# Kernel tuning notes

Measured on AMD Instinct MI355X. Metric: run time of the kernel, lower is better.

## Reference

```python
import jax, jax.numpy as jnp
import numpy as np

EPS_THRESH = 1e-10   # threshold used by GraphFilter to sparsify A
NORM_EPS = 1e-12     # torch F.normalize clamp
REG = 2.0 / 3.0      # AGE preprocess_graph reg coefficient (layer=1)


def setup_inputs() -> dict:
    key = jax.random.key(0)
    X = jax.random.normal(key, (8192, 512), dtype=jnp.float32)
    return {"X": X}


def reference(X):
    N = X.shape[0]
    # row L2-normalize (torch F.normalize semantics)
    norms = jnp.maximum(jnp.linalg.norm(X, axis=1, keepdims=True), NORM_EPS)
    feats = X / norms
    # dense cosine-similarity graph, thresholded at epsilon
    A = feats @ feats.T                               # [N, N]
    A = jnp.where(A < EPS_THRESH, 0.0, A)
    # remove self-loops (adj - diag_sparse in the original)
    idx = jnp.arange(N)
    A = A.at[idx, idx].set(0.0)
    # preprocess_graph(norm='sym', renorm=True): adj_ = A + I, sym-normalize
    rowsum = jnp.sum(A, axis=1) + 1.0                 # diag of (A + I)
    d_inv_sqrt = rowsum ** -0.5
    A_norm = A * d_inv_sqrt[:, None] * d_inv_sqrt[None, :]
    # A+I normalized: off-diag from A_norm, diag contributes d_i^-1
    diag_term = d_inv_sqrt * d_inv_sqrt               # = 1/rowsum
    # filter = I - reg * (I - (A_norm + diag(diag_term)))
    #        = (1-reg) I + reg * (A_norm + diag(diag_term))
    # propagate: out = filter @ X
    out = (1.0 - REG) * X + REG * (A_norm @ X + (diag_term[:, None] * X))
    return out
```

## Files before the change

### kernel.cpp

```cpp
#include <hip/hip_runtime.h>


#define NR 8192
#define DC 512
#define KZN 4

typedef unsigned short u16;
typedef signed char i8;
typedef float f32x4 __attribute__((ext_vector_type(4)));
typedef int i32x4 __attribute__((ext_vector_type(4)));
typedef u16 u16x4 __attribute__((ext_vector_type(4)));

#define QF_INV 453.5714285f
#define DEQA   4.8608093e-6f
#define QS_INV 254.0f
#define QY_INV 211.6666666f
#define DEQ    1.8600229e-5f

__device__ __forceinline__ float bf2f(u16 u) {
  union { unsigned u; float f; } v; v.u = ((unsigned)u) << 16; return v.f;
}
__device__ __forceinline__ u16 f2bf(float f) {
  union { float f; unsigned u; } v; v.f = f;
  unsigned r = v.u + 0x7fffu + ((v.u >> 16) & 1u);
  return (u16)(r >> 16);
}

__device__ __forceinline__ void async16(const void* ga, void* la) {
  __builtin_amdgcn_global_load_lds(
      (const __attribute__((address_space(1))) unsigned int*)ga,
      (__attribute__((address_space(3))) unsigned int*)la, 16, 0, 0);
}

template <int ROWS, int NT>
__device__ __forceinline__ void stage_i8_k128(const i8* __restrict__ g, int ld,
                                              int row0, int k0, i8* lds, int tid) {
  constexpr int PER = (ROWS * 8) / NT;
#pragma unroll
  for (int q = 0; q < PER; ++q) {
    int s = q * NT + tid;
    int r = s >> 3;
    int kq = (s & 7) ^ (r & 7);
    async16(g + (size_t)(row0 + r) * ld + (k0 + kq * 16), lds + s * 16);
  }
}
__device__ __forceinline__ i32x4 frag_i8_k128(const i8* lds, int m, int c) {
  int phys = c ^ (m & 7);
  return *(const i32x4*)(lds + m * 128 + phys * 16);
}

__global__ __launch_bounds__(256) void k_normalize(const float* __restrict__ X,
                                                   i8* __restrict__ F) {
  int row = blockIdx.x;
  int tid = threadIdx.x;
  const float* xr = X + (size_t)row * DC;
  float2 v = *(const float2*)(xr + 2 * tid);
  float s = v.x * v.x + v.y * v.y;
#pragma unroll
  for (int off = 32; off; off >>= 1) s += __shfl_down(s, off);
  __shared__ float wsum[4];
  if ((tid & 63) == 0) wsum[tid >> 6] = s;
  __syncthreads();
  float tot = wsum[0] + wsum[1] + wsum[2] + wsum[3];
  float scale = QF_INV / fmaxf(sqrtf(tot), 1e-12f);
  int q0 = (int)rintf(v.x * scale);
  int q1 = (int)rintf(v.y * scale);
  q0 = q0 > 127 ? 127 : (q0 < -127 ? -127 : q0);
  q1 = q1 > 127 ? 127 : (q1 < -127 ? -127 : q1);
  u16 pk = (u16)((q0 & 255) | ((q1 & 255) << 8));
  ((u16*)(F + (size_t)row * DC))[tid] = pk;
}

__global__ __launch_bounds__(256, 4) void k_simgemm(const i8* __restrict__ F,
                                                    i8* __restrict__ S,
                                                    float* __restrict__ rs_mat) {
  __shared__ alignas(16) char smem[32768];
  i8* As = (i8*)smem;
  i8* Bs = (i8*)(smem + 16384);
  int tid = threadIdx.x, lane = tid & 63, wave = tid >> 6;
  int b = blockIdx.x;
  int tj = (int)((sqrtf(8.f * b + 1.f) - 1.f) * 0.5f);
  while ((tj + 1) * (tj + 2) / 2 <= b) ++tj;
  while (tj * (tj + 1) / 2 > b) --tj;
  int ti = b - tj * (tj + 1) / 2;
  bool diag = (ti == tj);

  int wm = wave >> 1, wn = wave & 1;
  int quad = lane >> 4, col = lane & 15;
  i32x4 zero = {0, 0, 0, 0};
  i32x4 acc[4][4];
#pragma unroll
  for (int a = 0; a < 4; ++a)
#pragma unroll
    for (int c = 0; c < 4; ++c) acc[a][c] = zero;

  const i8* Bsrc = diag ? As : Bs;
  for (int kt = 0; kt < DC; kt += 128) {
    __syncthreads();
    stage_i8_k128<128, 256>(F, DC, ti * 128, kt, As, tid);
    if (!diag) stage_i8_k128<128, 256>(F, DC, tj * 128, kt, Bs, tid);
    __syncthreads();
#pragma unroll
    for (int kc = 0; kc < 2; ++kc) {
      i32x4 af[4], bfr[4];
#pragma unroll
      for (int mi = 0; mi < 4; ++mi)
        af[mi] = frag_i8_k128(As, wm * 64 + mi * 16 + col, kc * 4 + quad);
#pragma unroll
      for (int ni = 0; ni < 4; ++ni)
        bfr[ni] = frag_i8_k128(Bsrc, wn * 64 + ni * 16 + col, kc * 4 + quad);
#pragma unroll
      for (int mi = 0; mi < 4; ++mi)
#pragma unroll
        for (int ni = 0; ni < 4; ++ni)
          acc[mi][ni] = __builtin_amdgcn_mfma_i32_16x16x64_i8(af[mi], bfr[ni], acc[mi][ni], 0, 0, 0);
    }
  }

  int av[4][4][4];
  int csI[4] = {0, 0, 0, 0};
  int rvI[16];
#pragma unroll
  for (int u = 0; u < 16; ++u) rvI[u] = 0;
#pragma unroll
  for (int mi = 0; mi < 4; ++mi) {
#pragma unroll
    for (int r = 0; r < 4; ++r) {
      int gi = ti * 128 + wm * 64 + mi * 16 + quad * 4 + r;
#pragma unroll
      for (int ni = 0; ni < 4; ++ni) {
        int gj = tj * 128 + wn * 64 + ni * 16 + col;
        int a = acc[mi][ni][r];
        a = a > 0 ? a : 0;
        if (diag && gi == gj) a = 0;
        av[mi][ni][r] = a;
        csI[ni] += a;
        rvI[mi * 4 + r] += a;
      }
    }
  }
#pragma unroll
  for (int ni = 0; ni < 4; ++ni) {
    int c = csI[ni];
    c += __shfl_xor(c, 16);
    c += __shfl_xor(c, 32);
    if (quad == 0) {
      int gj = tj * 128 + wn * 64 + ni * 16 + col;
      rs_mat[((size_t)ti * 2 + wm) * NR + gj] = (float)c * DEQA;
    }
  }
  if (!diag) {
#pragma unroll
    for (int u = 0; u < 16; ++u) {
      int c = rvI[u];
      c += __shfl_xor(c, 1);
      c += __shfl_xor(c, 2);
      c += __shfl_xor(c, 4);
      c += __shfl_xor(c, 8);
      if (col == 0) {
        int mi = u >> 2, r = u & 3;
        int gi = ti * 128 + wm * 64 + mi * 16 + quad * 4 + r;
        rs_mat[((size_t)tj * 2 + wn) * NR + gi] = (float)c * DEQA;
      }
    }
  }

  char* direct = smem;
  char* mirror = smem + 16384;
  __syncthreads();
#pragma unroll
  for (int mi = 0; mi < 4; ++mi) {
#pragma unroll
    for (int ni = 0; ni < 4; ++ni) {
      int cg = wn * 64 + ni * 16 + col;
      int q[4];
#pragma unroll
      for (int r = 0; r < 4; ++r) {
        float avf = (float)av[mi][ni][r] * DEQA;
        int qq = (int)rintf(avf * QS_INV);
        q[r] = qq > 127 ? 127 : qq;
      }
#pragma unroll
      for (int r = 0; r < 4; ++r) {
        int row = wm * 64 + mi * 16 + quad * 4 + r;
        int chunk = (cg >> 4) ^ (row & 7);
        direct[row * 128 + chunk * 16 + (cg & 15)] = (char)q[r];
      }
      if (!diag) {
        int mcb = wm * 64 + mi * 16 + quad * 4;
        int chunk = (mcb >> 4) ^ (cg & 7);
        unsigned pk = (unsigned)(q[0] & 255) | ((unsigned)(q[1] & 255) << 8) |
                      ((unsigned)(q[2] & 255) << 16) | ((unsigned)(q[3] & 255) << 24);
        *(unsigned*)(mirror + cg * 128 + chunk * 16 + (mcb & 15)) = pk;
      }
    }
  }
  __syncthreads();
  {
    int r2 = tid >> 1, half = tid & 1;
#pragma unroll
    for (int k = 0; k < 4; ++k) {
      int c = half * 4 + k;
      int phys = c ^ (r2 & 7);
      i32x4 d = *(const i32x4*)(direct + r2 * 128 + phys * 16);
      *(i32x4*)(S + (size_t)(ti * 128 + r2) * NR + tj * 128 + c * 16) = d;
    }
    if (!diag) {
#pragma unroll
      for (int k = 0; k < 4; ++k) {
        int c = half * 4 + k;
        int phys = c ^ (r2 & 7);
        i32x4 d = *(const i32x4*)(mirror + r2 * 128 + phys * 16);
        *(i32x4*)(S + (size_t)(tj * 128 + r2) * NR + ti * 128 + c * 16) = d;
      }
    }
  }
}

__global__ __launch_bounds__(128) void k_rs(const float* __restrict__ rs_mat,
                                            float* __restrict__ rsum1) {
  int i = blockIdx.x * 128 + threadIdx.x;
  float s = 1.0f;
#pragma unroll
  for (int k = 0; k < 128; ++k) s += rs_mat[(size_t)k * NR + i];
  rsum1[i] = s;
}

__global__ __launch_bounds__(256) void k_make_yt(const float* __restrict__ X,
                                                 const float* __restrict__ rsum1,
                                                 i8* __restrict__ Yt) {
  __shared__ float T[64][65];
  int i0 = blockIdx.x * 64, k0 = blockIdx.y * 64;
  int tid = threadIdx.x;
  {
    int iL = tid >> 2, ks = (tid & 3) * 4;
    const float* xr = X + (size_t)(i0 + iL) * DC + k0;
#pragma unroll
    for (int u = 0; u < 4; ++u) {
      float4 f = *(const float4*)(xr + ks + u * 16);
      T[iL][ks + u * 16 + 0] = f.x;
      T[iL][ks + u * 16 + 1] = f.y;
      T[iL][ks + u * 16 + 2] = f.z;
      T[iL][ks + u * 16 + 3] = f.w;
    }
  }
  __syncthreads();
  {
    int kL = tid >> 2, ib = (tid & 3) * 16;
    char pk[16];
#pragma unroll
    for (int u = 0; u < 16; ++u) {
      float dj = rsqrtf(rsum1[i0 + ib + u]);
      float v = T[ib + u][kL] * dj;
      int q = (int)rintf(v * QY_INV);
      q = q > 127 ? 127 : (q < -127 ? -127 : q);
      pk[u] = (char)q;
    }
    *(i32x4*)(Yt + (size_t)(k0 + kL) * NR + i0 + ib) = *(const i32x4*)pk;
  }
}

__global__ __launch_bounds__(512, 2) void k_outgemm(const i8* __restrict__ S,
                                                    const i8* __restrict__ Yt,
                                                    u16* __restrict__ Pb) {
  __shared__ alignas(16) i8 As[128 * 128];
  __shared__ alignas(16) i8 Ys[512 * 128];
  int tid = threadIdx.x, lane = tid & 63, wave = tid >> 6;
  int ti = blockIdx.x, kz = blockIdx.y;
  int wm = wave & 1, wn = wave >> 1;
  int quad = lane >> 4, col = lane & 15;
  i32x4 zero = {0, 0, 0, 0};
  i32x4 acc[4][8];
#pragma unroll
  for (int a = 0; a < 4; ++a)
#pragma unroll
    for (int c = 0; c < 8; ++c) acc[a][c] = zero;

  const int KCH = NR / KZN;
  int k_lo = kz * KCH, k_hi = k_lo + KCH;
  for (int kt = k_lo; kt < k_hi; kt += 128) {
    __syncthreads();
    stage_i8_k128<128, 512>(S, NR, ti * 128, kt, As, tid);
    stage_i8_k128<512, 512>(Yt, NR, 0, kt, Ys, tid);
    __syncthreads();
#pragma unroll
    for (int kc = 0; kc < 2; ++kc) {
      i32x4 af[4], bfr[8];
#pragma unroll
      for (int mi = 0; mi < 4; ++mi)
        af[mi] = frag_i8_k128(As, wm * 64 + mi * 16 + col, kc * 4 + quad);
#pragma unroll
      for (int ni = 0; ni < 8; ++ni)
        bfr[ni] = frag_i8_k128(Ys, wn * 128 + ni * 16 + col, kc * 4 + quad);
#pragma unroll
      for (int mi = 0; mi < 4; ++mi)
#pragma unroll
        for (int ni = 0; ni < 8; ++ni)
          acc[mi][ni] = __builtin_amdgcn_mfma_i32_16x16x64_i8(af[mi], bfr[ni], acc[mi][ni], 0, 0, 0);
    }
  }
#pragma unroll
  for (int mi = 0; mi < 4; ++mi) {
#pragma unroll
    for (int r = 0; r < 4; ++r) {
      int gi = ti * 128 + wm * 64 + mi * 16 + quad * 4 + r;
#pragma unroll
      for (int ni = 0; ni < 8; ++ni) {
        int gj = wn * 128 + ni * 16 + col;
        Pb[((size_t)kz * NR + gi) * DC + gj] = f2bf((float)acc[mi][ni][r] * DEQ);
      }
    }
  }
}

__global__ __launch_bounds__(256) void k_reduce(const u16* __restrict__ Pb,
                                               const float* __restrict__ X,
                                               const float* __restrict__ rsum1,
                                               float* __restrict__ out) {
  const float c1 = (float)(2.0 / 3.0);
  const float c0 = 1.0f - c1;
  size_t idx = ((size_t)blockIdx.x * 256 + threadIdx.x) * 4;
  int i = (int)(idx >> 9);
  float4 s = {0.f, 0.f, 0.f, 0.f};
#pragma unroll
  for (int kz = 0; kz < KZN; ++kz) {
    u16x4 p = *(const u16x4*)(Pb + (size_t)kz * NR * DC + idx);
    s.x += bf2f(p[0]); s.y += bf2f(p[1]); s.z += bf2f(p[2]); s.w += bf2f(p[3]);
  }
  float4 x = *(const float4*)(X + idx);
  float rs = rsum1[i];
  float sc = c1 * rsqrtf(rs);
  float xs = c0 + c1 / rs;
  float4 o = {xs * x.x + sc * s.x, xs * x.y + sc * s.y,
              xs * x.z + sc * s.z, xs * x.w + sc * s.w};
  *(float4*)(out + idx) = o;
}

extern "C" void kernel_launch(void* const* d_in, const int* in_sizes, int n_in,
                              void* d_out, int out_size, void* d_ws, size_t ws_size,
                              hipStream_t stream) {
  const float* X = (const float*)d_in[0];
  float* out = (float*)d_out;
  char* ws = (char*)d_ws;
  i8*  S  = (i8*)(ws);
  i8*  F  = (i8*)(ws + 67108864);
  i8*  Yt = (i8*)(ws + 71303168);
  float* rsum1  = (float*)(ws + 75497472);
  u16* Pb = (u16*)(ws + 75530240);
  float* rs_mat = (float*)(ws + 75530240);

  k_normalize<<<dim3(NR), dim3(256), 0, stream>>>(X, F);
  k_simgemm<<<dim3(64 * 65 / 2), dim3(256), 0, stream>>>(F, S, rs_mat);
  k_rs<<<dim3(64), dim3(128), 0, stream>>>(rs_mat, rsum1);
  k_make_yt<<<dim3(128, 8), dim3(256), 0, stream>>>(X, rsum1, Yt);
  k_outgemm<<<dim3(64, KZN), dim3(512), 0, stream>>>(S, Yt, Pb);
  k_reduce<<<dim3(NR * DC / 1024), dim3(256), 0, stream>>>(Pb, X, rsum1, out);
}
```

Baseline: 221.8 us.

## Enlarge similarity GEMM tiles to 256x256 with 512 threads per block

The symmetric int8 similarity GEMM moves from 128x128 tiles with 256 threads to 256x256 tiles with 512 threads, halving the number of triangular blocks and raising operand reuse per staged byte. Diagonal tiles now stage B separately, and the mirrored transpose write reuses a single 64KB LDS buffer after an extra barrier. Row and column partial sums go to separate buffers that are zeroed with a memset so that k_rs can sum them. In exchange it uses more LDS and registers per block, allows fewer resident blocks, and adds a memset launch.

```diff
diff --git a/kernel.cpp b/kernel.cpp
--- a/kernel.cpp
+++ b/kernel.cpp
@@ -71,12 +71,13 @@
   ((u16*)(F + (size_t)row * DC))[tid] = pk;
 }
 
-__global__ __launch_bounds__(256, 4) void k_simgemm(const i8* __restrict__ F,
+__global__ __launch_bounds__(512, 2) void k_simgemm(const i8* __restrict__ F,
                                                     i8* __restrict__ S,
-                                                    float* __restrict__ rs_mat) {
-  __shared__ alignas(16) char smem[32768];
+                                                    float* __restrict__ rs_cmat,
+                                                    float* __restrict__ rs_rmat) {
+  __shared__ alignas(16) char smem[65536];
   i8* As = (i8*)smem;
-  i8* Bs = (i8*)(smem + 16384);
+  i8* Bs = (i8*)(smem + 32768);
   int tid = threadIdx.x, lane = tid & 63, wave = tid >> 6;
   int b = blockIdx.x;
   int tj = (int)((sqrtf(8.f * b + 1.f) - 1.f) * 0.5f);
@@ -85,55 +86,53 @@
   int ti = b - tj * (tj + 1) / 2;
   bool diag = (ti == tj);
 
-  int wm = wave >> 1, wn = wave & 1;
+  int wm = wave >> 2, wn = wave & 3;
   int quad = lane >> 4, col = lane & 15;
   i32x4 zero = {0, 0, 0, 0};
-  i32x4 acc[4][4];
-#pragma unroll
-  for (int a = 0; a < 4; ++a)
+  i32x4 acc[8][4];
+#pragma unroll
+  for (int a = 0; a < 8; ++a)
 #pragma unroll
     for (int c = 0; c < 4; ++c) acc[a][c] = zero;
 
-  const i8* Bsrc = diag ? As : Bs;
   for (int kt = 0; kt < DC; kt += 128) {
     __syncthreads();
-    stage_i8_k128<128, 256>(F, DC, ti * 128, kt, As, tid);
-    if (!diag) stage_i8_k128<128, 256>(F, DC, tj * 128, kt, Bs, tid);
+    stage_i8_k128<256, 512>(F, DC, ti * 256, kt, As, tid);
+    stage_i8_k128<256, 512>(F, DC, tj * 256, kt, Bs, tid);
     __syncthreads();
 #pragma unroll
     for (int kc = 0; kc < 2; ++kc) {
-      i32x4 af[4], bfr[4];
-#pragma unroll
-      for (int mi = 0; mi < 4; ++mi)
-        af[mi] = frag_i8_k128(As, wm * 64 + mi * 16 + col, kc * 4 + quad);
+      i32x4 af[8], bfr[4];
+#pragma unroll
+      for (int mi = 0; mi < 8; ++mi)
+        af[mi] = frag_i8_k128(As, wm * 128 + mi * 16 + col, kc * 4 + quad);
 #pragma unroll
       for (int ni = 0; ni < 4; ++ni)
-        bfr[ni] = frag_i8_k128(Bsrc, wn * 64 + ni * 16 + col, kc * 4 + quad);
-#pragma unroll
-      for (int mi = 0; mi < 4; ++mi)
+        bfr[ni] = frag_i8_k128(Bs, wn * 64 + ni * 16 + col, kc * 4 + quad);
+#pragma unroll
+      for (int mi = 0; mi < 8; ++mi)
 #pragma unroll
         for (int ni = 0; ni < 4; ++ni)
           acc[mi][ni] = __builtin_amdgcn_mfma_i32_16x16x64_i8(af[mi], bfr[ni], acc[mi][ni], 0, 0, 0);
     }
   }
 
-  int av[4][4][4];
   int csI[4] = {0, 0, 0, 0};
-  int rvI[16];
-#pragma unroll
-  for (int u = 0; u < 16; ++u) rvI[u] = 0;
-#pragma unroll
-  for (int mi = 0; mi < 4; ++mi) {
+  int rvI[32];
+#pragma unroll
+  for (int u = 0; u < 32; ++u) rvI[u] = 0;
+#pragma unroll
+  for (int mi = 0; mi < 8; ++mi) {
 #pragma unroll
     for (int r = 0; r < 4; ++r) {
-      int gi = ti * 128 + wm * 64 + mi * 16 + quad * 4 + r;
+      int gi = ti * 256 + wm * 128 + mi * 16 + quad * 4 + r;
 #pragma unroll
       for (int ni = 0; ni < 4; ++ni) {
-        int gj = tj * 128 + wn * 64 + ni * 16 + col;
+        int gj = tj * 256 + wn * 64 + ni * 16 + col;
         int a = acc[mi][ni][r];
         a = a > 0 ? a : 0;
         if (diag && gi == gj) a = 0;
-        av[mi][ni][r] = a;
+        acc[mi][ni][r] = a;
         csI[ni] += a;
         rvI[mi * 4 + r] += a;
       }
@@ -145,13 +144,13 @@
     c += __shfl_xor(c, 16);
     c += __shfl_xor(c, 32);
     if (quad == 0) {
-      int gj = tj * 128 + wn * 64 + ni * 16 + col;
-      rs_mat[((size_t)ti * 2 + wm) * NR + gj] = (float)c * DEQA;
+      int gj = tj * 256 + wn * 64 + ni * 16 + col;
+      rs_cmat[((size_t)ti * 2 + wm) * NR + gj] = (float)c * DEQA;
     }
   }
   if (!diag) {
 #pragma unroll
-    for (int u = 0; u < 16; ++u) {
+    for (int u = 0; u < 32; ++u) {
       int c = rvI[u];
       c += __shfl_xor(c, 1);
       c += __shfl_xor(c, 2);
@@ -159,39 +158,27 @@
       c += __shfl_xor(c, 8);
       if (col == 0) {
         int mi = u >> 2, r = u & 3;
-        int gi = ti * 128 + wm * 64 + mi * 16 + quad * 4 + r;
-        rs_mat[((size_t)tj * 2 + wn) * NR + gi] = (float)c * DEQA;
-      }
-    }
-  }
-
-  char* direct = smem;
-  char* mirror = smem + 16384;
+        int gi = ti * 256 + wm * 128 + mi * 16 + quad * 4 + r;
+        rs_rmat[((size_t)tj * 4 + wn) * NR + gi] = (float)c * DEQA;
+      }
+    }
+  }
+
+  char* buf = smem;
   __syncthreads();
 #pragma unroll
-  for (int mi = 0; mi < 4; ++mi) {
+  for (int mi = 0; mi < 8; ++mi) {
 #pragma unroll
     for (int ni = 0; ni < 4; ++ni) {
       int cg = wn * 64 + ni * 16 + col;
-      int q[4];
 #pragma unroll
       for (int r = 0; r < 4; ++r) {
-        float avf = (float)av[mi][ni][r] * DEQA;
-        int qq = (int)rintf(avf * QS_INV);
-        q[r] = qq > 127 ? 127 : qq;
-      }
-#pragma unroll
-      for (int r = 0; r < 4; ++r) {
-        int row = wm * 64 + mi * 16 + quad * 4 + r;
-        int chunk = (cg >> 4) ^ (row & 7);
-        direct[row * 128 + chunk * 16 + (cg & 15)] = (char)q[r];
-      }
-      if (!diag) {
-        int mcb = wm * 64 + mi * 16 + quad * 4;
-        int chunk = (mcb >> 4) ^ (cg & 7);
-        unsigned pk = (unsigned)(q[0] & 255) | ((unsigned)(q[1] & 255) << 8) |
-                      ((unsigned)(q[2] & 255) << 16) | ((unsigned)(q[3] & 255) << 24);
-        *(unsigned*)(mirror + cg * 128 + chunk * 16 + (mcb & 15)) = pk;
+        int a = acc[mi][ni][r];
+        int qq = (int)rintf((float)a * (DEQA * QS_INV));
+        qq = qq > 127 ? 127 : qq;
+        int row = wm * 128 + mi * 16 + quad * 4 + r;
+        int chunk = (cg >> 4) ^ (row & 15);
+        buf[row * 256 + chunk * 16 + (cg & 15)] = (char)qq;
       }
     }
   }
@@ -199,30 +186,57 @@
   {
     int r2 = tid >> 1, half = tid & 1;
 #pragma unroll
-    for (int k = 0; k < 4; ++k) {
-      int c = half * 4 + k;
-      int phys = c ^ (r2 & 7);
-      i32x4 d = *(const i32x4*)(direct + r2 * 128 + phys * 16);
-      *(i32x4*)(S + (size_t)(ti * 128 + r2) * NR + tj * 128 + c * 16) = d;
-    }
-    if (!diag) {
-#pragma unroll
-      for (int k = 0; k < 4; ++k) {
-        int c = half * 4 + k;
-        int phys = c ^ (r2 & 7);
-        i32x4 d = *(const i32x4*)(mirror + r2 * 128 + phys * 16);
-        *(i32x4*)(S + (size_t)(tj * 128 + r2) * NR + ti * 128 + c * 16) = d;
-      }
-    }
-  }
-}
-
-__global__ __launch_bounds__(128) void k_rs(const float* __restrict__ rs_mat,
+    for (int k = 0; k < 8; ++k) {
+      int c = half * 8 + k;
+      int phys = c ^ (r2 & 15);
+      i32x4 d = *(const i32x4*)(buf + r2 * 256 + phys * 16);
+      *(i32x4*)(S + (size_t)(ti * 256 + r2) * NR + tj * 256 + c * 16) = d;
+    }
+  }
+  if (!diag) {
+    __syncthreads();
+#pragma unroll
+    for (int mi = 0; mi < 8; ++mi) {
+#pragma unroll
+      for (int ni = 0; ni < 4; ++ni) {
+        int cg = wn * 64 + ni * 16 + col;
+        int q[4];
+#pragma unroll
+        for (int r = 0; r < 4; ++r) {
+          int a = acc[mi][ni][r];
+          int qq = (int)rintf((float)a * (DEQA * QS_INV));
+          q[r] = qq > 127 ? 127 : qq;
+        }
+        int mcb = wm * 128 + mi * 16 + quad * 4;
+        int chunk = (mcb >> 4) ^ (cg & 15);
+        unsigned pk = (unsigned)(q[0] & 255) | ((unsigned)(q[1] & 255) << 8) |
+                      ((unsigned)(q[2] & 255) << 16) | ((unsigned)(q[3] & 255) << 24);
+        *(unsigned*)(buf + cg * 256 + chunk * 16 + (mcb & 15)) = pk;
+      }
+    }
+    __syncthreads();
+    {
+      int r2 = tid >> 1, half = tid & 1;
+#pragma unroll
+      for (int k = 0; k < 8; ++k) {
+        int c = half * 8 + k;
+        int phys = c ^ (r2 & 15);
+        i32x4 d = *(const i32x4*)(buf + r2 * 256 + phys * 16);
+        *(i32x4*)(S + (size_t)(tj * 256 + r2) * NR + ti * 256 + c * 16) = d;
+      }
+    }
+  }
+}
+
+__global__ __launch_bounds__(128) void k_rs(const float* __restrict__ rs_cmat,
+                                            const float* __restrict__ rs_rmat,
                                             float* __restrict__ rsum1) {
   int i = blockIdx.x * 128 + threadIdx.x;
   float s = 1.0f;
 #pragma unroll
-  for (int k = 0; k < 128; ++k) s += rs_mat[(size_t)k * NR + i];
+  for (int k = 0; k < 64; ++k) s += rs_cmat[(size_t)k * NR + i];
+#pragma unroll
+  for (int k = 0; k < 128; ++k) s += rs_rmat[(size_t)k * NR + i];
   rsum1[i] = s;
 }
 
@@ -347,11 +361,13 @@
   i8*  Yt = (i8*)(ws + 71303168);
   float* rsum1  = (float*)(ws + 75497472);
   u16* Pb = (u16*)(ws + 75530240);
-  float* rs_mat = (float*)(ws + 75530240);
+  float* rs_cmat = (float*)(ws + 75530240);
+  float* rs_rmat = (float*)(ws + 75530240 + 2097152);
 
   k_normalize<<<dim3(NR), dim3(256), 0, stream>>>(X, F);
-  k_simgemm<<<dim3(64 * 65 / 2), dim3(256), 0, stream>>>(F, S, rs_mat);
-  k_rs<<<dim3(64), dim3(128), 0, stream>>>(rs_mat, rsum1);
+  hipMemsetAsync(ws + 75530240, 0, 6291456, stream);
+  k_simgemm<<<dim3(32 * 33 / 2), dim3(512), 0, stream>>>(F, S, rs_cmat, rs_rmat);
+  k_rs<<<dim3(64), dim3(128), 0, stream>>>(rs_cmat, rs_rmat, rsum1);
   k_make_yt<<<dim3(128, 8), dim3(256), 0, stream>>>(X, rsum1, Yt);
   k_outgemm<<<dim3(64, KZN), dim3(512), 0, stream>>>(S, Yt, Pb);
   k_reduce<<<dim3(NR * DC / 1024), dim3(256), 0, stream>>>(Pb, X, rsum1, out);
```

Result: slower. 258.9 us (+16.7%).
